# Kernel tuning notes

Measured on AMD Instinct MI355X. Metric: run time of the kernel, lower is better.

## Reference

```python
import jax, jax.numpy as jnp
import numpy as np

NEG_SLOPE = 0.2
EPS = 1e-16


def setup_inputs() -> dict:
    N, E, IN, H, C = 100000, 1600000, 128, 4, 16
    key = jax.random.key(0)
    k1, k2, k3, k4, k5 = jax.random.split(key, 5)
    x = jax.random.normal(k1, (N, IN), dtype=jnp.float32)
    edge_index = jax.random.randint(k2, (2, E), 0, N, dtype=jnp.int64)
    # Xavier-uniform init like nn.init.xavier_uniform_
    limW = float(np.sqrt(6.0 / (IN + H * C)))
    W = jax.random.uniform(k3, (IN, H * C), dtype=jnp.float32, minval=-limW, maxval=limW)
    lima = float(np.sqrt(6.0 / (H + C)))
    att = jax.random.uniform(k4, (1, H, C), dtype=jnp.float32, minval=-lima, maxval=lima)
    bias = jnp.zeros((H * C,), dtype=jnp.float32)
    return {"x": x, "edge_index": edge_index, "W": W, "att": att, "bias": bias}


def reference(x, edge_index, W, att, bias):
    N = x.shape[0]
    H, C = att.shape[1], att.shape[2]
    h = (x @ W).reshape(N, H, C)  # [N,H,C]
    # add self loops
    loops = jnp.arange(N, dtype=edge_index.dtype)
    row = jnp.concatenate([edge_index[0], loops])  # target nodes
    col = jnp.concatenate([edge_index[1], loops])  # source nodes
    x_i = h[row]  # [Etot,H,C]
    x_j = h[col]
    e = jax.nn.leaky_relu(x_i + x_j, NEG_SLOPE)
    alpha = jnp.einsum('ehc,hc->eh', e, att[0])  # [Etot,H]
    # segment softmax keyed by row (every node has a self loop -> no empty segments)
    amax = jax.lax.stop_gradient(jax.ops.segment_max(alpha, row, num_segments=N))
    ea = jnp.exp(alpha - amax[row])
    denom = jax.ops.segment_sum(ea, row, num_segments=N)
    alpha = ea / (denom[row] + EPS)
    # weighted message scatter-add (dropout p=0 / eval mode)
    out = jax.ops.segment_sum(x_j * alpha[:, :, None], row, num_segments=N)  # [N,H,C]
    out = out.reshape(N, H * C) + bias  # concat=True
    return out
```

## Files before the change

kernel.cpp:

```cpp
#include <hip/hip_runtime.h>

#define NEG_SLOPE 0.2f

typedef float f32x2 __attribute__((ext_vector_type(2)));
typedef float f32x4 __attribute__((ext_vector_type(4)));
typedef short bf16x8 __attribute__((ext_vector_type(8)));

__device__ __forceinline__ unsigned short f2bf(float f) {
  union { float f; unsigned u; } v; v.f = f;
  unsigned r = v.u + 0x7fff + ((v.u >> 16) & 1);
  return (unsigned short)(r >> 16);
}
__device__ __forceinline__ float bf2f(unsigned short u) {
  union { unsigned u; float f; } v; v.u = ((unsigned)u) << 16;
  return v.f;
}
__device__ __forceinline__ unsigned pkbf(float a, float b) {
  return (unsigned)f2bf(a) | ((unsigned)f2bf(b) << 16);
}
__device__ __forceinline__ f32x4 upk4(uint2 u) {
  union { unsigned u; float f; } a, b, c, d;
  a.u = u.x << 16; b.u = u.x & 0xffff0000u;
  c.u = u.y << 16; d.u = u.y & 0xffff0000u;
  f32x4 r; r.x = a.f; r.y = b.f; r.z = c.f; r.w = d.f;
  return r;
}

__global__ __launch_bounds__(256) void gemm_mfma(const float* __restrict__ x,
                                                 const float* __restrict__ W,
                                                 unsigned short* __restrict__ hb, int N) {
  __shared__ uint4 Bl[1024];
  const int t = threadIdx.x;
  {
    const int l = t & 63;
    const int kt = (t >> 6) & 3;
    const int kb = kt * 32 + ((l >> 4) * 8);
    const int cb = l & 15;
#pragma unroll
    for (int ct = 0; ct < 4; ct++) {
      const float* wp = W + (size_t)kb * 64 + ct * 16 + cb;
      unsigned p[4];
#pragma unroll
      for (int jj = 0; jj < 4; jj++)
        p[jj] = pkbf(wp[(2 * jj) * 64], wp[(2 * jj + 1) * 64]);
      Bl[(ct * 4 + kt) * 64 + l] = make_uint4(p[0], p[1], p[2], p[3]);
    }
  }
  __syncthreads();
  const int l = t & 63;
  const int wv = t >> 6;
  union BU { bf16x8 v; uint4 q; };
  BU b[4][4];
#pragma unroll
  for (int ct = 0; ct < 4; ct++)
#pragma unroll
    for (int kt = 0; kt < 4; kt++) b[ct][kt].q = Bl[(ct * 4 + kt) * 64 + l];

  const int rowbase0 = blockIdx.x * 256 + wv * 64;
#pragma unroll
  for (int rt = 0; rt < 4; rt++) {
    const int rbase = rowbase0 + rt * 16;
    int rl = rbase + (l & 15);
    if (rl >= N) rl = N - 1;
    const float* xp = x + (size_t)rl * 128 + ((l >> 4) * 8);
    BU ah[4], alo[4];
#pragma unroll
    for (int kt = 0; kt < 4; kt++) {
      float f[8];
      float4 v0 = *(const float4*)(xp + kt * 32);
      float4 v1 = *(const float4*)(xp + kt * 32 + 4);
      f[0] = v0.x; f[1] = v0.y; f[2] = v0.z; f[3] = v0.w;
      f[4] = v1.x; f[5] = v1.y; f[6] = v1.z; f[7] = v1.w;
      unsigned short hs[8], ls[8];
#pragma unroll
      for (int j = 0; j < 8; j++) {
        hs[j] = f2bf(f[j]);
        ls[j] = f2bf(f[j] - bf2f(hs[j]));
      }
      ah[kt].q = make_uint4(hs[0] | (hs[1] << 16), hs[2] | (hs[3] << 16),
                            hs[4] | (hs[5] << 16), hs[6] | (hs[7] << 16));
      alo[kt].q = make_uint4(ls[0] | (ls[1] << 16), ls[2] | (ls[3] << 16),
                             ls[4] | (ls[5] << 16), ls[6] | (ls[7] << 16));
    }
#pragma unroll
    for (int ct = 0; ct < 4; ct++) {
      f32x4 acc = {0.f, 0.f, 0.f, 0.f};
#pragma unroll
      for (int kt = 0; kt < 4; kt++) {
        acc = __builtin_amdgcn_mfma_f32_16x16x32_bf16(ah[kt].v, b[ct][kt].v, acc, 0, 0, 0);
        acc = __builtin_amdgcn_mfma_f32_16x16x32_bf16(alo[kt].v, b[ct][kt].v, acc, 0, 0, 0);
      }
#pragma unroll
      for (int j = 0; j < 4; j++) {
        float v = acc[j];
        float pv = __shfl_xor(v, 1);
        int row = rbase + (l >> 4) * 4 + j;
        if (!(l & 1) && row < N) {
          *(unsigned*)((char*)hb + (size_t)row * 128 + ct * 32 + (l & 15) * 2) =
              pkbf(v, pv);
        }
      }
    }
  }
}

#define TILE 4096
#define EPT 16
#define NBKT_MAX 256

__global__ __launch_bounds__(256) void bucket_pass(const int* __restrict__ rowi,
                                                   const int* __restrict__ coli,
                                                   int* __restrict__ bucket_fill,
                                                   unsigned* __restrict__ bucket_arr,
                                                   int E, int Cedge, int Ctot, int NBKT) {
  __shared__ int cnt[NBKT_MAX];
  __shared__ int base[NBKT_MAX];
  const int t = threadIdx.x;
  const int tile0 = blockIdx.x * TILE;
  for (int i = t; i < NBKT_MAX; i += 256) cnt[i] = 0;
  __syncthreads();
  unsigned pk[EPT];
  int bk[EPT];
#pragma unroll
  for (int j = 0; j < EPT; j++) {
    int i = tile0 + j * 256 + t;
    if (i < E) {
      int r = rowi[i];
      int c = coli[i];
      bk[j] = r >> 9;
      pk[j] = ((unsigned)(r & 511) << 17) | (unsigned)c;
      atomicAdd(&cnt[bk[j]], 1);
    } else {
      bk[j] = -1;
    }
  }
  __syncthreads();
  if (t < NBKT) {
    int n = cnt[t];
    base[t] = (n > 0) ? atomicAdd(&bucket_fill[t], n) : 0;
    cnt[t] = 0;
  }
  __syncthreads();
#pragma unroll
  for (int j = 0; j < EPT; j++) {
    if (bk[j] >= 0) {
      int lp = atomicAdd(&cnt[bk[j]], 1);
      int pos = base[bk[j]] + lp;
      if (pos < Cedge) bucket_arr[bk[j] * Ctot + pos] = pk[j];
    }
  }
}

#define STAGE_CAP 10240

__global__ __launch_bounds__(256) void csr_pass(unsigned* __restrict__ bucket_arr,
                                                const int* __restrict__ bucket_fill,
                                                int2* __restrict__ rowinfo,
                                                int Cedge, int Ctot, int N) {
  __shared__ unsigned stage[STAGE_CAP];
  __shared__ int hist[512], excl[512], pairs[256];
  const int t = threadIdx.x;
  const int b = blockIdx.x;
  const int bb = b * Ctot;
  const int r0 = b << 9;
  const int nb = min(bucket_fill[b], Cedge);
  for (int i = t; i < 512; i += 256) hist[i] = ((r0 + i) < N) ? 1 : 0;
  for (int i = t; i < nb; i += 256) stage[i] = bucket_arr[bb + i];
  __syncthreads();
  for (int i = t; i < nb; i += 256) atomicAdd(&hist[stage[i] >> 17], 1);
  __syncthreads();
  int h0 = hist[2 * t], h1 = hist[2 * t + 1];
  int ps = h0 + h1;
  pairs[t] = ps;
  __syncthreads();
  for (int off = 1; off < 256; off <<= 1) {
    int val = pairs[t] + ((t >= off) ? pairs[t - off] : 0);
    __syncthreads();
    pairs[t] = val;
    __syncthreads();
  }
  int pexcl = pairs[t] - ps;
  excl[2 * t] = pexcl;
  excl[2 * t + 1] = pexcl + h0;
  __syncthreads();
  for (int r = t; r < 512; r += 256) {
    int gr = r0 + r;
    if (gr < N) {
      int o = bb + excl[r];
      rowinfo[gr] = make_int2(o, o + hist[r]);
    }
  }
  __syncthreads();
  for (int i = t; i < nb; i += 256) {
    unsigned pk = stage[i];
    int r = pk >> 17;
    int lp = atomicAdd(&excl[r], 1);
    bucket_arr[bb + lp] = (pk & 0x1FFFFu) << 7;
  }
  __syncthreads();
  for (int r = t; r < 512; r += 256) {
    int gr = r0 + r;
    if (gr < N) bucket_arr[bb + excl[r]] = (unsigned)gr << 7;
  }
}

#define ESTEP(u)                                        \
  {                                                     \
    f32x4 jv = upk4(u);                                 \
    f32x4 s = hiv + jv;                                 \
    f32x4 as;                                           \
    as.x = fabsf(s.x); as.y = fabsf(s.y);               \
    as.z = fabsf(s.z); as.w = fabsf(s.w);               \
    f32x4 d = s * attA + as * attB;                     \
    float al = (d.x + d.y) + (d.z + d.w);               \
    al += __shfl_xor(al, 1);                            \
    al += __shfl_xor(al, 2);                            \
    float p = __expf(al);                               \
    acc += jv * p;                                      \
    den += p;                                           \
  }

__global__ __launch_bounds__(256) void node_pass(const unsigned short* __restrict__ hb,
                                                 const int2* __restrict__ rowinfo,
                                                 const unsigned* __restrict__ srcs,
                                                 const float* __restrict__ att,
                                                 const float* __restrict__ bias,
                                                 float* __restrict__ out, int N) {
  int w = (blockIdx.x * blockDim.x + threadIdx.x) >> 6;
  if (w >= N) return;
  const int lane = threadIdx.x & 63;
  const int lr = lane & 15;
  const int q = lane >> 4;
  const char* hbc = (const char*)hb;
  const unsigned loff = (unsigned)(lr << 3);
  const f32x4 attv = *(const f32x4*)(att + 4 * lr);
  const f32x4 attA = attv * 0.6f;
  const f32x4 attB = attv * 0.4f;
  const int2 oi = rowinfo[w];
  int k = oi.x;
  const int k1 = oi.y;
  const f32x4 hiv = upk4(*(const uint2*)(hbc + (((unsigned)w << 7) | loff)));
  f32x4 acc = {0.f, 0.f, 0.f, 0.f};
  float den = 0.f;
  for (; k + 16 <= k1; k += 16) {
    unsigned o0 = srcs[k + q] | loff;
    unsigned o1 = srcs[k + 4 + q] | loff;
    unsigned o2 = srcs[k + 8 + q] | loff;
    unsigned o3 = srcs[k + 12 + q] | loff;
    uint2 u0 = *(const uint2*)(hbc + o0);
    uint2 u1 = *(const uint2*)(hbc + o1);
    uint2 u2 = *(const uint2*)(hbc + o2);
    uint2 u3 = *(const uint2*)(hbc + o3);
    ESTEP(u0);
    ESTEP(u1);
    ESTEP(u2);
    ESTEP(u3);
  }
  for (; k + 4 <= k1; k += 4) {
    unsigned o = srcs[k + q] | loff;
    uint2 u = *(const uint2*)(hbc + o);
    ESTEP(u);
  }
  if (k < k1) {
    int kk = k + q;
    bool act = kk < k1;
    unsigned o = (act ? srcs[kk] : srcs[k]) | loff;
    uint2 u = *(const uint2*)(hbc + o);
    f32x4 jv = upk4(u);
    f32x4 s = hiv + jv;
    f32x4 as;
    as.x = fabsf(s.x); as.y = fabsf(s.y);
    as.z = fabsf(s.z); as.w = fabsf(s.w);
    f32x4 d = s * attA + as * attB;
    float al = (d.x + d.y) + (d.z + d.w);
    al += __shfl_xor(al, 1);
    al += __shfl_xor(al, 2);
    float p = act ? __expf(al) : 0.f;
    acc += jv * p;
    den += p;
  }
  acc.x += __shfl_xor(acc.x, 16); acc.y += __shfl_xor(acc.y, 16);
  acc.z += __shfl_xor(acc.z, 16); acc.w += __shfl_xor(acc.w, 16);
  den += __shfl_xor(den, 16);
  acc.x += __shfl_xor(acc.x, 32); acc.y += __shfl_xor(acc.y, 32);
  acc.z += __shfl_xor(acc.z, 32); acc.w += __shfl_xor(acc.w, 32);
  den += __shfl_xor(den, 32);
  if (q == 0) {
    float inv = 1.0f / (den + 1e-16f);
    f32x4 bv = *(const f32x4*)(bias + 4 * lr);
    f32x4 o = acc * inv + bv;
    *(f32x4*)(out + (size_t)w * 64 + 4 * lr) = o;
  }
}

extern "C" void kernel_launch(void* const* d_in, const int* in_sizes, int n_in,
                              void* d_out, int out_size, void* d_ws, size_t ws_size,
                              hipStream_t stream) {
  const float* x = (const float*)d_in[0];
  const int* eidx = (const int*)d_in[1];
  const float* W = (const float*)d_in[2];
  const float* att = (const float*)d_in[3];
  const float* bias = (const float*)d_in[4];
  float* out = (float*)d_out;

  const int N = in_sizes[0] / 128;
  const int E = in_sizes[1] / 2;
  const int NBKT = (N + 511) >> 9;
  int Cedge = (E + NBKT - 1) / NBKT;
  Cedge = Cedge + Cedge / 8 + 64;
  Cedge = (Cedge + 15) & ~15;
  if (Cedge > STAGE_CAP) Cedge = STAGE_CAP;
  const int Ctot = Cedge + 512;

  unsigned short* hb = (unsigned short*)d_ws;
  int* bucket_fill = (int*)(hb + (size_t)N * 64);
  int2* rowinfo = (int2*)(bucket_fill + NBKT_MAX);
  unsigned* bucket_arr = (unsigned*)(rowinfo + N);

  hipMemsetAsync(bucket_fill, 0, NBKT_MAX * sizeof(int), stream);

  gemm_mfma<<<(N + 255) / 256, 256, 0, stream>>>(x, W, hb, N);
  bucket_pass<<<(E + TILE - 1) / TILE, 256, 0, stream>>>(eidx, eidx + E, bucket_fill,
                                                         bucket_arr, E, Cedge, Ctot, NBKT);
  csr_pass<<<NBKT, 256, 0, stream>>>(bucket_arr, bucket_fill, rowinfo, Cedge, Ctot, N);
  node_pass<<<(N * 64 + 255) / 256, 256, 0, stream>>>(hb, rowinfo, bucket_arr, att, bias,
                                                      out, N);
}
```

Baseline: 115.7 us.

## Widen node_pass loads to 8 channels per lane, stage bucket scatter in LDS

```diff
diff --git a/kernel.cpp b/kernel.cpp
--- a/kernel.cpp
+++ b/kernel.cpp
@@ -2,7 +2,6 @@
 
 #define NEG_SLOPE 0.2f
 
-typedef float f32x2 __attribute__((ext_vector_type(2)));
 typedef float f32x4 __attribute__((ext_vector_type(4)));
 typedef short bf16x8 __attribute__((ext_vector_type(8)));
 
@@ -18,12 +17,23 @@
 __device__ __forceinline__ unsigned pkbf(float a, float b) {
   return (unsigned)f2bf(a) | ((unsigned)f2bf(b) << 16);
 }
-__device__ __forceinline__ f32x4 upk4(uint2 u) {
+__device__ __forceinline__ f32x4 upk4(unsigned ux, unsigned uy) {
   union { unsigned u; float f; } a, b, c, d;
-  a.u = u.x << 16; b.u = u.x & 0xffff0000u;
-  c.u = u.y << 16; d.u = u.y & 0xffff0000u;
+  a.u = ux << 16; b.u = ux & 0xffff0000u;
+  c.u = uy << 16; d.u = uy & 0xffff0000u;
   f32x4 r; r.x = a.f; r.y = b.f; r.z = c.f; r.w = d.f;
   return r;
+}
+__device__ __forceinline__ f32x4 absfma(f32x4 s, f32x4 coef, f32x4 d) {
+  d.x = fmaf(fabsf(s.x), coef.x, d.x);
+  d.y = fmaf(fabsf(s.y), coef.y, d.y);
+  d.z = fmaf(fabsf(s.z), coef.z, d.z);
+  d.w = fmaf(fabsf(s.w), coef.w, d.w);
+  return d;
+}
+__device__ __forceinline__ float dpp_xor1_add(float x) {
+  int y = __builtin_amdgcn_mov_dpp(__builtin_bit_cast(int, x), 0xB1, 0xF, 0xF, true);
+  return x + __builtin_bit_cast(float, y);
 }
 
 __global__ __launch_bounds__(256) void gemm_mfma(const float* __restrict__ x,
@@ -114,10 +124,15 @@
                                                    unsigned* __restrict__ bucket_arr,
                                                    int E, int Cedge, int Ctot, int NBKT) {
   __shared__ int cnt[NBKT_MAX];
-  __shared__ int base[NBKT_MAX];
+  __shared__ int excl[NBKT_MAX];
+  __shared__ int gadj[NBKT_MAX];
+  __shared__ int tmp[NBKT_MAX];
+  __shared__ unsigned staged[TILE];
+  __shared__ unsigned char bkof[TILE];
   const int t = threadIdx.x;
   const int tile0 = blockIdx.x * TILE;
-  for (int i = t; i < NBKT_MAX; i += 256) cnt[i] = 0;
+  const int nt = min(TILE, E - tile0);
+  cnt[t] = 0;
   __syncthreads();
   unsigned pk[EPT];
   int bk[EPT];
@@ -135,19 +150,35 @@
     }
   }
   __syncthreads();
-  if (t < NBKT) {
-    int n = cnt[t];
-    base[t] = (n > 0) ? atomicAdd(&bucket_fill[t], n) : 0;
-    cnt[t] = 0;
-  }
+  int v = cnt[t];
+  tmp[t] = v;
+  __syncthreads();
+  for (int off = 1; off < 256; off <<= 1) {
+    int val = tmp[t] + ((t >= off) ? tmp[t - off] : 0);
+    __syncthreads();
+    tmp[t] = val;
+    __syncthreads();
+  }
+  int ex = tmp[t] - v;
+  excl[t] = ex;
+  int ga = 0;
+  if (v > 0) ga = atomicAdd(&bucket_fill[t], v);
+  gadj[t] = ga - ex;
+  cnt[t] = ex;
   __syncthreads();
 #pragma unroll
   for (int j = 0; j < EPT; j++) {
     if (bk[j] >= 0) {
       int lp = atomicAdd(&cnt[bk[j]], 1);
-      int pos = base[bk[j]] + lp;
-      if (pos < Cedge) bucket_arr[bk[j] * Ctot + pos] = pk[j];
-    }
+      staged[lp] = pk[j];
+      bkof[lp] = (unsigned char)bk[j];
+    }
+  }
+  __syncthreads();
+  for (int i = t; i < nt; i += 256) {
+    int b = bkof[i];
+    int pb = i + gadj[b];
+    if (pb < Cedge) bucket_arr[b * Ctot + pb] = staged[i];
   }
 }
 
@@ -204,20 +235,21 @@
   }
 }
 
-#define ESTEP(u)                                        \
-  {                                                     \
-    f32x4 jv = upk4(u);                                 \
-    f32x4 s = hiv + jv;                                 \
-    f32x4 as;                                           \
-    as.x = fabsf(s.x); as.y = fabsf(s.y);               \
-    as.z = fabsf(s.z); as.w = fabsf(s.w);               \
-    f32x4 d = s * attA + as * attB;                     \
-    float al = (d.x + d.y) + (d.z + d.w);               \
-    al += __shfl_xor(al, 1);                            \
-    al += __shfl_xor(al, 2);                            \
-    float p = __expf(al);                               \
-    acc += jv * p;                                      \
-    den += p;                                           \
+#define ESTEP8(u, gate)                                  \
+  {                                                      \
+    f32x4 ja = upk4((u).x, (u).y);                       \
+    f32x4 jb = upk4((u).z, (u).w);                       \
+    f32x4 sa = hia + ja, sb = hib + jb;                  \
+    f32x4 da = sa * attAa, db = sb * attAb;              \
+    da = absfma(sa, attBa, da);                          \
+    db = absfma(sb, attBb, db);                          \
+    float al = ((da.x + da.y) + (da.z + da.w)) +         \
+               ((db.x + db.y) + (db.z + db.w));          \
+    al = dpp_xor1_add(al);                               \
+    float p = (gate) ? __expf(al) : 0.f;                 \
+    acca += ja * p;                                      \
+    accb += jb * p;                                      \
+    den += p;                                            \
   }
 
 __global__ __launch_bounds__(256) void node_pass(const unsigned short* __restrict__ hb,
@@ -229,67 +261,63 @@
   int w = (blockIdx.x * blockDim.x + threadIdx.x) >> 6;
   if (w >= N) return;
   const int lane = threadIdx.x & 63;
-  const int lr = lane & 15;
-  const int q = lane >> 4;
+  const int lr = lane & 7;
+  const int s = lane >> 3;
   const char* hbc = (const char*)hb;
-  const unsigned loff = (unsigned)(lr << 3);
-  const f32x4 attv = *(const f32x4*)(att + 4 * lr);
-  const f32x4 attA = attv * 0.6f;
-  const f32x4 attB = attv * 0.4f;
+  const unsigned loff = (unsigned)(lr << 4);
+  const f32x4 attAa = *(const f32x4*)(att + 8 * lr) * 0.6f;
+  const f32x4 attAb = *(const f32x4*)(att + 8 * lr + 4) * 0.6f;
+  const f32x4 attBa = *(const f32x4*)(att + 8 * lr) * 0.4f;
+  const f32x4 attBb = *(const f32x4*)(att + 8 * lr + 4) * 0.4f;
   const int2 oi = rowinfo[w];
   int k = oi.x;
   const int k1 = oi.y;
-  const f32x4 hiv = upk4(*(const uint2*)(hbc + (((unsigned)w << 7) | loff)));
-  f32x4 acc = {0.f, 0.f, 0.f, 0.f};
+  uint4 hv = *(const uint4*)(hbc + (((unsigned)w << 7) | loff));
+  const f32x4 hia = upk4(hv.x, hv.y);
+  const f32x4 hib = upk4(hv.z, hv.w);
+  f32x4 acca = {0.f, 0.f, 0.f, 0.f};
+  f32x4 accb = {0.f, 0.f, 0.f, 0.f};
   float den = 0.f;
   for (; k + 16 <= k1; k += 16) {
-    unsigned o0 = srcs[k + q] | loff;
-    unsigned o1 = srcs[k + 4 + q] | loff;
-    unsigned o2 = srcs[k + 8 + q] | loff;
-    unsigned o3 = srcs[k + 12 + q] | loff;
-    uint2 u0 = *(const uint2*)(hbc + o0);
-    uint2 u1 = *(const uint2*)(hbc + o1);
-    uint2 u2 = *(const uint2*)(hbc + o2);
-    uint2 u3 = *(const uint2*)(hbc + o3);
-    ESTEP(u0);
-    ESTEP(u1);
-    ESTEP(u2);
-    ESTEP(u3);
-  }
-  for (; k + 4 <= k1; k += 4) {
-    unsigned o = srcs[k + q] | loff;
-    uint2 u = *(const uint2*)(hbc + o);
-    ESTEP(u);
+    unsigned o0 = srcs[k + s] | loff;
+    unsigned o1 = srcs[k + 8 + s] | loff;
+    uint4 u0 = *(const uint4*)(hbc + o0);
+    uint4 u1 = *(const uint4*)(hbc + o1);
+    ESTEP8(u0, true);
+    ESTEP8(u1, true);
+  }
+  for (; k + 8 <= k1; k += 8) {
+    unsigned o = srcs[k + s] | loff;
+    uint4 u = *(const uint4*)(hbc + o);
+    ESTEP8(u, true);
   }
   if (k < k1) {
-    int kk = k + q;
-    bool act = kk < k1;
-    unsigned o = (act ? srcs[kk] : srcs[k]) | loff;
-    uint2 u = *(const uint2*)(hbc + o);
-    f32x4 jv = upk4(u);
-    f32x4 s = hiv + jv;
-    f32x4 as;
-    as.x = fabsf(s.x); as.y = fabsf(s.y);
-    as.z = fabsf(s.z); as.w = fabsf(s.w);
-    f32x4 d = s * attA + as * attB;
-    float al = (d.x + d.y) + (d.z + d.w);
-    al += __shfl_xor(al, 1);
-    al += __shfl_xor(al, 2);
-    float p = act ? __expf(al) : 0.f;
-    acc += jv * p;
-    den += p;
-  }
-  acc.x += __shfl_xor(acc.x, 16); acc.y += __shfl_xor(acc.y, 16);
-  acc.z += __shfl_xor(acc.z, 16); acc.w += __shfl_xor(acc.w, 16);
+    bool act = (k + s) < k1;
+    unsigned o = (act ? srcs[k + s] : srcs[k]) | loff;
+    uint4 u = *(const uint4*)(hbc + o);
+    ESTEP8(u, act);
+  }
+#pragma unroll
+  for (int j = 0; j < 4; j++) {
+    acca[j] += __shfl_xor(acca[j], 8);
+    accb[j] += __shfl_xor(accb[j], 8);
+    acca[j] += __shfl_xor(acca[j], 16);
+    accb[j] += __shfl_xor(accb[j], 16);
+    acca[j] += __shfl_xor(acca[j], 32);
+    accb[j] += __shfl_xor(accb[j], 32);
+  }
+  den += __shfl_xor(den, 8);
   den += __shfl_xor(den, 16);
-  acc.x += __shfl_xor(acc.x, 32); acc.y += __shfl_xor(acc.y, 32);
-  acc.z += __shfl_xor(acc.z, 32); acc.w += __shfl_xor(acc.w, 32);
   den += __shfl_xor(den, 32);
-  if (q == 0) {
+  if (s == 0) {
     float inv = 1.0f / (den + 1e-16f);
-    f32x4 bv = *(const f32x4*)(bias + 4 * lr);
-    f32x4 o = acc * inv + bv;
-    *(f32x4*)(out + (size_t)w * 64 + 4 * lr) = o;
+    f32x4 bva = *(const f32x4*)(bias + 8 * lr);
+    f32x4 bvb = *(const f32x4*)(bias + 8 * lr + 4);
+    f32x4 oa = acca * inv + bva;
+    f32x4 ob = accb * inv + bvb;
+    float* op = out + (size_t)w * 64 + 8 * lr;
+    *(f32x4*)op = oa;
+    *(f32x4*)(op + 4) = ob;
   }
 }
 
```

New measurement: 124.3 us. 7.4% more time.
